# Optimization experiments

Measured on AMD Instinct MI355X. Metric: run time of the kernel, lower is better.

Reference implementation:

```python
import jax, jax.numpy as jnp
import numpy as np
import math

GROUPS = 32
EPS = 1e-5

def group_norm(x, w, b):
    B, C, H, W = x.shape
    xg = x.reshape(B, GROUPS, C // GROUPS, H, W)
    mu = xg.mean(axis=(2, 3, 4), keepdims=True)
    var = xg.var(axis=(2, 3, 4), keepdims=True)
    xn = ((xg - mu) * jax.lax.rsqrt(var + EPS)).reshape(B, C, H, W)
    return xn * w[None, :, None, None] + b[None, :, None, None]

def conv1x1(x, w, b):
    # x: [B,Cin,H,W], w: [Cout,Cin], b: [Cout]
    return jnp.einsum('bchw,oc->bohw', x, w) + b[None, :, None, None]

def setup_inputs() -> dict:
    key = jax.random.key(0)
    ks = jax.random.split(key, 8)
    B, C, E, H, W = 8, 256, 512, 64, 64
    x = jax.random.normal(ks[0], (B, C, H, W), dtype=jnp.float32)
    condA = jax.random.normal(ks[1], (B, E, H, W), dtype=jnp.float32)
    gn_x_w = jnp.ones((C,), jnp.float32)
    gn_x_b = jnp.zeros((C,), jnp.float32)
    gn_c_w = jnp.ones((E,), jnp.float32)
    gn_c_b = jnp.zeros((E,), jnp.float32)
    q_w = jax.random.normal(ks[2], (C, C), jnp.float32) * 0.02
    q_b = jnp.zeros((C,), jnp.float32)
    k_w = jax.random.normal(ks[3], (C, E), jnp.float32) * 0.02
    k_b = jnp.zeros((C,), jnp.float32)
    v_w = jax.random.normal(ks[4], (C, E), jnp.float32) * 0.02
    v_b = jnp.zeros((C,), jnp.float32)
    return {"x": x, "condA": condA, "gn_x_w": gn_x_w, "gn_x_b": gn_x_b,
            "gn_c_w": gn_c_w, "gn_c_b": gn_c_b, "q_w": q_w, "q_b": q_b,
            "k_w": k_w, "k_b": k_b, "v_w": v_w, "v_b": v_b}

def reference(x, condA, gn_x_w, gn_x_b, gn_c_w, gn_c_b, q_w, q_b, k_w, k_b, v_w, v_b):
    B, C, H, W = x.shape
    scale = math.sqrt(C)
    h = group_norm(x, gn_x_w, gn_x_b)
    h1 = group_norm(condA, gn_c_w, gn_c_b)
    q = conv1x1(h, q_w, q_b)      # [B,C,H,W]
    k = conv1x1(h1, k_w, k_b)     # [B,C,Hc,Wc]
    v = conv1x1(h1, v_w, v_b)     # [B,C,Hc,Wc]
    qf = q.transpose(0, 2, 3, 1).reshape(B, H * W, C)        # [B,N,C]
    kf = k.reshape(B, C, -1)                                  # [B,C,M]
    vf = v.transpose(0, 2, 3, 1).reshape(B, -1, C)            # [B,M,C]
    attn = jax.nn.softmax(jnp.einsum('bnc,bcm->bnm', qf, kf) / scale, axis=-1)
    out = jnp.einsum('bnm,bmc->bnc', attn, vf)                # [B,N,C]
    return out.reshape(B, H, W, C).transpose(0, 3, 1, 2)
```

## Files before the change

### kernel.cpp

```cpp
#include <hip/hip_runtime.h>


typedef _Float16 half8 __attribute__((ext_vector_type(8)));
typedef _Float16 half4v __attribute__((ext_vector_type(4)));
typedef float f32x4 __attribute__((ext_vector_type(4)));
typedef float f32x16 __attribute__((ext_vector_type(16)));

#define MFMA16(a, b, c) __builtin_amdgcn_mfma_f32_16x16x32_f16((a), (b), (c), 0, 0, 0)
#define MFMA32(a, b, c) __builtin_amdgcn_mfma_f32_32x32x16_f16((a), (b), (c), 0, 0, 0)

__global__ __launch_bounds__(256) void statswconv_kernel(
    const float* __restrict__ x, const float* __restrict__ condA,
    float* __restrict__ sx, float* __restrict__ sc,
    const float* __restrict__ wq, const float* __restrict__ wk,
    const float* __restrict__ wv, _Float16* __restrict__ wqt,
    _Float16* __restrict__ wkt, _Float16* __restrict__ wvt) {
  int bid = blockIdx.x;
  int t = threadIdx.x;
  if (bid >= 512) {
    int i = (bid - 512) * 256 + t;
    const float* src;
    _Float16* dst;
    int cin, ksbits, gi;
    if (i < 8192) { src = wq; dst = wqt; cin = 256; ksbits = 3; gi = i; }
    else if (i < 24576) { src = wk; dst = wkt; cin = 512; ksbits = 4; gi = i - 8192; }
    else { src = wv; dst = wvt; cin = 512; ksbits = 4; gi = i - 24576; }
    int tile = gi >> 6, g = gi & 63;
    int otile = tile >> ksbits, ks = tile & ((1 << ksbits) - 1);
    int o = otile * 16 + (g & 15), k = ks * 32 + (g >> 4) * 8;
    const float* s = src + (size_t)o * cin + k;
    half8 hv;
#pragma unroll
    for (int j = 0; j < 8; j++) hv[j] = (_Float16)s[j];
    *(half8*)(dst + (size_t)gi * 8) = hv;
    return;
  }
  const float4* src;
  int nf4;
  float* dst;
  float inv_n;
  if (bid < 256) {
    src = (const float4*)(x + (size_t)bid * 32768);
    nf4 = 8192;
    dst = sx + bid * 2;
    inv_n = 1.0f / 32768.0f;
  } else {
    int j = bid - 256;
    src = (const float4*)(condA + (size_t)j * 65536);
    nf4 = 16384;
    dst = sc + j * 2;
    inv_n = 1.0f / 65536.0f;
  }
  float s = 0.f, s2 = 0.f;
  for (int i = t; i < nf4; i += 256) {
    float4 v = src[i];
    s += v.x + v.y + v.z + v.w;
    s2 += v.x * v.x + v.y * v.y + v.z * v.z + v.w * v.w;
  }
#pragma unroll
  for (int m = 1; m <= 32; m <<= 1) {
    s += __shfl_xor(s, m, 64);
    s2 += __shfl_xor(s2, m, 64);
  }
  __shared__ float red[8];
  int w = t >> 6;
  if ((t & 63) == 0) { red[w * 2] = s; red[w * 2 + 1] = s2; }
  __syncthreads();
  if (t == 0) {
    float S = red[0] + red[2] + red[4] + red[6];
    float S2 = red[1] + red[3] + red[5] + red[7];
    float mu = S * inv_n;
    float var = S2 * inv_n - mu * mu;
    dst[0] = mu;
    dst[1] = rsqrtf(var + 1e-5f);
  }
}

__global__ __launch_bounds__(256) void ntrans_kernel(
    const float* __restrict__ x, const float* __restrict__ condA,
    const float* __restrict__ statsx, const float* __restrict__ statsc,
    const float* __restrict__ gxw, const float* __restrict__ gxb,
    const float* __restrict__ gcw, const float* __restrict__ gcb,
    _Float16* __restrict__ hxTt, _Float16* __restrict__ h1Tt) {
  int bid = blockIdx.x;
  const float *src, *stats, *gw, *gb;
  _Float16* dst;
  int CH, gsh, bid2;
  if (bid < 2048) {
    src = x; stats = statsx; gw = gxw; gb = gxb; dst = hxTt;
    CH = 256; gsh = 3; bid2 = bid;
  } else {
    src = condA; stats = statsc; gw = gcw; gb = gcb; dst = h1Tt;
    CH = 512; gsh = 4; bid2 = bid - 2048;
  }
  int b = bid2 & 7, nt = (bid2 >> 3) & 63, ctile = bid2 >> 9;
  int n0 = nt * 64, c0 = ctile * 64;
  int t = threadIdx.x;
  __shared__ float tile[64][65];

  int cl = t >> 2;
  int c = c0 + cl;
  const float* st = stats + ((size_t)b * 32 + (c >> gsh)) * 2;
  float mu = st[0], rs = st[1];
  float a = rs * gw[c];
  float bb = gb[c] - mu * a;
  const float* srow = src + ((size_t)(b * CH + c)) * 4096 + n0 + (t & 3) * 16;
#pragma unroll
  for (int i = 0; i < 4; i++) {
    float4 v = *(const float4*)(srow + 4 * i);
    int nn = (t & 3) * 16 + 4 * i;
    tile[cl][nn + 0] = v.x * a + bb;
    tile[cl][nn + 1] = v.y * a + bb;
    tile[cl][nn + 2] = v.z * a + bb;
    tile[cl][nn + 3] = v.w * a + bb;
  }
  __syncthreads();
  int nl = t >> 2;
  half8 ov[2];
#pragma unroll
  for (int u = 0; u < 2; u++)
#pragma unroll
    for (int i = 0; i < 8; i++) ov[u][i] = (_Float16)tile[(t & 3) * 16 + 8 * u + i][nl];
  int n = n0 + nl;
  size_t tb = ((size_t)b * 256 + (n >> 4)) * (CH >> 5);
  int ca = c0 + (t & 3) * 16;
#pragma unroll
  for (int u = 0; u < 2; u++) {
    int cc = ca + 8 * u;
    size_t addr = ((tb + (cc >> 5)) * 64 + (n & 15) + 16 * ((cc >> 3) & 3)) * 8;
    *(half8*)(dst + addr) = ov[u];
  }
}

__global__ __launch_bounds__(256, 2) void projQ_kernel(
    const _Float16* __restrict__ Ht, const _Float16* __restrict__ Wt,
    const float* __restrict__ bias, _Float16* __restrict__ Qt) {
  int bid = blockIdx.x;
  int b = bid & 7, nt = bid >> 3;
  int t = threadIdx.x, l = t & 63, w = t >> 6;
  int c15 = l & 15, q = l >> 4;

  __shared__ __align__(16) _Float16 hbuf[16384];
  half8* hb = (half8*)hbuf;
  {
    const half8* sg = (const half8*)Ht + (size_t)(b * 256 + nt * 4) * 512;
#pragma unroll
    for (int i = 0; i < 8; i++) hb[t + 256 * i] = sg[t + 256 * i];
  }
  __syncthreads();

  const half8* wt8 = (const half8*)Wt;
#pragma unroll
  for (int p = 0; p < 2; p++) {
    int oa = (p * 4 + w) * 2;
    f32x4 acc[2][4] = {};
#pragma unroll
    for (int ks = 0; ks < 8; ks++) {
      half8 af0 = wt8[((size_t)(oa + 0) * 8 + ks) * 64 + l];
      half8 af1 = wt8[((size_t)(oa + 1) * 8 + ks) * 64 + l];
#pragma unroll
      for (int nt2 = 0; nt2 < 4; nt2++) {
        half8 bf = hb[(nt2 * 8 + ks) * 64 + l];
        acc[0][nt2] = MFMA16(af0, bf, acc[0][nt2]);
        acc[1][nt2] = MFMA16(af1, bf, acc[1][nt2]);
      }
    }
#pragma unroll
    for (int j = 0; j < 2; j++) {
      int o4 = (oa + j) * 16 + 4 * q;
      f32x4 bv = *(const f32x4*)(bias + o4);
#pragma unroll
      for (int nt2 = 0; nt2 < 4; nt2++) {
        half4v hv;
#pragma unroll
        for (int r = 0; r < 4; r++) hv[r] = (_Float16)((acc[j][nt2][r] + bv[r]) * 0.0625f);
        size_t addr = ((((size_t)b * 128 + nt * 2 + (nt2 >> 1)) * 16 + (oa + j)) * 64 +
                       (nt2 & 1) * 16 + c15 + 32 * (q >> 1)) * 8 + (q & 1) * 4;
        *(half4v*)(Qt + addr) = hv;
      }
    }
  }
}

__global__ __launch_bounds__(256, 2) void projKV_kernel(
    const _Float16* __restrict__ Ht, const _Float16* __restrict__ Wk,
    const _Float16* __restrict__ Wv, const float* __restrict__ kb,
    const float* __restrict__ vb, _Float16* __restrict__ Kt,
    _Float16* __restrict__ Vt) {
  int bid = blockIdx.x;
  int b = bid & 7, mt = bid >> 3;
  int m0 = mt * 64;
  int t = threadIdx.x, l = t & 63, w = t >> 6;
  int c15 = l & 15, q = l >> 4;

  __shared__ __align__(16) _Float16 hbuf[32768];
  half8* hb = (half8*)hbuf;
  {
    const half8* sg = (const half8*)Ht + (size_t)(b * 256 + mt * 4) * 1024;
#pragma unroll
    for (int i = 0; i < 16; i++) hb[t + 256 * i] = sg[t + 256 * i];
  }
  __syncthreads();

  const half8* wk8 = (const half8*)Wk;
  const half8* wv8 = (const half8*)Wv;
#pragma unroll
  for (int p = 0; p < 2; p++) {
    int oa = (p * 4 + w) * 2;
    f32x4 acck[2][4] = {};
    f32x4 accv[4][2] = {};
#pragma unroll
    for (int ks = 0; ks < 16; ks++) {
      half8 kf0 = wk8[((size_t)(oa + 0) * 16 + ks) * 64 + l];
      half8 kf1 = wk8[((size_t)(oa + 1) * 16 + ks) * 64 + l];
      half8 vf0 = wv8[((size_t)(oa + 0) * 16 + ks) * 64 + l];
      half8 vf1 = wv8[((size_t)(oa + 1) * 16 + ks) * 64 + l];
#pragma unroll
      for (int nt2 = 0; nt2 < 4; nt2++) {
        half8 lf = hb[(nt2 * 16 + ks) * 64 + l];
        acck[0][nt2] = MFMA16(kf0, lf, acck[0][nt2]);
        acck[1][nt2] = MFMA16(kf1, lf, acck[1][nt2]);
        accv[nt2][0] = MFMA16(lf, vf0, accv[nt2][0]);
        accv[nt2][1] = MFMA16(lf, vf1, accv[nt2][1]);
      }
    }
#pragma unroll
    for (int j = 0; j < 2; j++) {
      int o4 = (oa + j) * 16 + 4 * q;
      f32x4 bv = *(const f32x4*)(kb + o4);
#pragma unroll
      for (int nt2 = 0; nt2 < 4; nt2++) {
        half4v hv;
#pragma unroll
        for (int r = 0; r < 4; r++) hv[r] = (_Float16)(acck[j][nt2][r] + bv[r]);
        size_t addr = ((((size_t)b * 128 + mt * 2 + (nt2 >> 1)) * 16 + (oa + j)) * 64 +
                       (nt2 & 1) * 16 + c15 + 32 * (q >> 1)) * 8 + (q & 1) * 4;
        *(half4v*)(Kt + addr) = hv;
      }
    }
#pragma unroll
    for (int nt2 = 0; nt2 < 4; nt2++) {
      int m = m0 + nt2 * 16 + 4 * q;
      size_t mbase = ((size_t)b * 256 + (m >> 4)) * 8;
#pragma unroll
      for (int j = 0; j < 2; j++) {
        int c = (oa + j) * 16 + c15;
        float bs = vb[c];
        half4v hv;
#pragma unroll
        for (int r = 0; r < 4; r++) hv[r] = (_Float16)(accv[nt2][j][r] + bs);
        size_t addr = ((mbase + (c >> 5)) * 64 + (c & 31) + ((q >> 1) << 5)) * 8 + (q & 1) * 4;
        *(half4v*)(Vt + addr) = hv;
      }
    }
  }
}

__global__ __launch_bounds__(256, 2) void attn_kernel(
    const _Float16* __restrict__ Qt, const _Float16* __restrict__ Kt,
    const _Float16* __restrict__ Vt, float* __restrict__ out,
    float* __restrict__ O1, float* __restrict__ l0g,
    float* __restrict__ l1g) {
  int bid = blockIdx.x;
  int b = bid & 7, nt = (bid >> 3) & 63, ms = bid >> 9;
  int n0 = nt * 64;
  int t = threadIdx.x, l = t & 63, w = t >> 6;
  int l31 = l & 31, h = l >> 5;
  int mh = w & 1, nh = w >> 1;
  int it0 = ms * 32, it1 = it0 + 32;

  __shared__ __align__(16) _Float16 pbuf[8192];
  float* lsw = (float*)pbuf;

  half8 qf[16];
  {
    const half8* qt8 = (const half8*)Qt + ((size_t)(b * 128 + nt * 2 + nh) * 16) * 64 + l;
#pragma unroll
    for (int ks = 0; ks < 16; ks++) qf[ks] = qt8[ks * 64];
  }

  const half8* kt8 = (const half8*)Kt + (size_t)b * 131072 + (size_t)(mh * 16) * 64 + l;
  const half8* vt8 = (const half8*)Vt + (size_t)b * 131072 + l;
  int gb = (l31 ^ h) | (h << 5);

  f32x16 acc_o[4] = {};
  float l_part = 0.f;

  for (int it = it0; it < it1; it++) {
    _Float16* pb = pbuf + (it & 1) * 4096;

    half8 kfA[8];
#pragma unroll
    for (int i = 0; i < 8; i++) kfA[i] = kt8[(size_t)it * 2048 + i * 64];
    half8 vf0[8];
#pragma unroll
    for (int u = 0; u < 2; u++)
#pragma unroll
      for (int ct = 0; ct < 4; ct++)
        vf0[u * 4 + ct] = vt8[((size_t)(it * 4 + u) * 8 + (mh * 4 + ct)) * 64];

    f32x16 s = {};
    __builtin_amdgcn_s_setprio(1);
#pragma unroll
    for (int ks = 0; ks < 8; ks++) s = MFMA32(kfA[ks], qf[ks], s);
    __builtin_amdgcn_s_setprio(0);
    half8 kfB[8];
#pragma unroll
    for (int i = 0; i < 8; i++) kfB[i] = kt8[(size_t)it * 2048 + (8 + i) * 64];
    __builtin_amdgcn_s_setprio(1);
#pragma unroll
    for (int ks = 0; ks < 8; ks++) s = MFMA32(kfB[ks], qf[8 + ks], s);
    __builtin_amdgcn_s_setprio(0);

    half4v pv[4];
#pragma unroll
    for (int k2 = 0; k2 < 4; k2++) {
#pragma unroll
      for (int r = 0; r < 4; r++) {
        float e = __expf(s[4 * k2 + r]);
        l_part += e;
        pv[k2][r] = (_Float16)e;
      }
    }

#pragma unroll
    for (int k2 = 0; k2 < 4; k2++) {
      int hm = k2 & 1;
      int tau = nh * 4 + mh * 2 + (k2 >> 1);
      int g = (l31 ^ hm) | (hm << 5);
      *(half4v*)&pb[tau * 512 + g * 8 + 4 * h] = pv[k2];
    }
    __syncthreads();

    half8 vf1[8];
#pragma unroll
    for (int u = 0; u < 2; u++)
#pragma unroll
      for (int ct = 0; ct < 4; ct++)
        vf1[u * 4 + ct] = vt8[((size_t)(it * 4 + 2 + u) * 8 + (mh * 4 + ct)) * 64];
    __builtin_amdgcn_s_setprio(1);
#pragma unroll
    for (int ks = 0; ks < 2; ks++) {
      half8 pf = *(const half8*)&pb[(nh * 4 + ks) * 512 + gb * 8];
#pragma unroll
      for (int ct = 0; ct < 4; ct++) acc_o[ct] = MFMA32(pf, vf0[ks * 4 + ct], acc_o[ct]);
    }
#pragma unroll
    for (int ks = 2; ks < 4; ks++) {
      half8 pf = *(const half8*)&pb[(nh * 4 + ks) * 512 + gb * 8];
#pragma unroll
      for (int ct = 0; ct < 4; ct++) acc_o[ct] = MFMA32(pf, vf1[(ks - 2) * 4 + ct], acc_o[ct]);
    }
    __builtin_amdgcn_s_setprio(0);
  }

  __syncthreads();
  {
    float v = l_part + __shfl_xor(l_part, 32, 64);
    if (l < 32) lsw[mh * 64 + nh * 32 + l] = v;
  }
  __syncthreads();
  float* obase = ms ? O1 : out;
#pragma unroll
  for (int k2 = 0; k2 < 4; k2++) {
    int nb = nh * 32 + 4 * h + 8 * k2;
#pragma unroll
    for (int ct = 0; ct < 4; ct++) {
      int c = mh * 128 + ct * 32 + l31;
      f32x4 o4;
#pragma unroll
      for (int r = 0; r < 4; r++) o4[r] = acc_o[ct][4 * k2 + r];
      *(f32x4*)(obase + ((size_t)(b * 256 + c)) * 4096 + n0 + nb) = o4;
    }
  }
  if (t < 64) {
    float* lG = ms ? l1g : l0g;
    lG[b * 4096 + n0 + t] = lsw[t] + lsw[64 + t];
  }
}

__global__ __launch_bounds__(256) void combine_kernel(
    float* __restrict__ out, const float* __restrict__ O1,
    const float* __restrict__ l0g, const float* __restrict__ l1g) {
  size_t i = (size_t)blockIdx.x * 256 + threadIdx.x;
  f32x4 a = ((const f32x4*)out)[i];
  f32x4 b4 = ((const f32x4*)O1)[i];
  int bidx = (int)(i >> 18);
  int n4 = (int)(i & 1023);
  f32x4 La = ((const f32x4*)l0g)[bidx * 1024 + n4];
  f32x4 Lb = ((const f32x4*)l1g)[bidx * 1024 + n4];
  f32x4 r;
#pragma unroll
  for (int j = 0; j < 4; j++) r[j] = (a[j] + b4[j]) / (La[j] + Lb[j]);
  ((f32x4*)out)[i] = r;
}

extern "C" void kernel_launch(void* const* d_in, const int* in_sizes, int n_in,
                              void* d_out, int out_size, void* d_ws,
                              size_t ws_size, hipStream_t stream) {
  const float* x = (const float*)d_in[0];
  const float* condA = (const float*)d_in[1];
  const float* gxw = (const float*)d_in[2];
  const float* gxb = (const float*)d_in[3];
  const float* gcw = (const float*)d_in[4];
  const float* gcb = (const float*)d_in[5];
  const float* qw = (const float*)d_in[6];
  const float* qb = (const float*)d_in[7];
  const float* kw = (const float*)d_in[8];
  const float* kb = (const float*)d_in[9];
  const float* vw = (const float*)d_in[10];
  const float* vb = (const float*)d_in[11];
  float* out = (float*)d_out;

  char* ws = (char*)d_ws;
  float* statsx = (float*)(ws);
  float* statsc = (float*)(ws + 2048);
  _Float16* wqt = (_Float16*)(ws + 4096);
  _Float16* wkt = (_Float16*)(ws + 135168);
  _Float16* wvt = (_Float16*)(ws + 397312);
  char* p = ws + 659456;
  _Float16* hxTt = (_Float16*)p; p += (size_t)8 * 4096 * 256 * 2;
  _Float16* h1Tt = (_Float16*)p; p += (size_t)8 * 4096 * 512 * 2;
  _Float16* Qt = (_Float16*)p;   p += (size_t)8 * 4096 * 256 * 2;
  _Float16* Kt = (_Float16*)p;   p += (size_t)8 * 4096 * 256 * 2;
  _Float16* Vt = (_Float16*)p;

  float* O1 = (float*)(ws + 659456);
  float* l0g = (float*)(ws + 659456 + (size_t)33554432);
  float* l1g = (float*)(ws + 659456 + (size_t)33554432 + 131072);

  statswconv_kernel<<<672, 256, 0, stream>>>(x, condA, statsx, statsc,
                                             qw, kw, vw, wqt, wkt, wvt);
  ntrans_kernel<<<6144, 256, 0, stream>>>(x, condA, statsx, statsc,
                                          gxw, gxb, gcw, gcb, hxTt, h1Tt);
  projQ_kernel<<<512, 256, 0, stream>>>(hxTt, wqt, qb, Qt);
  projKV_kernel<<<512, 256, 0, stream>>>(h1Tt, wkt, wvt, kb, vb, Kt, Vt);
  attn_kernel<<<1024, 256, 0, stream>>>(Qt, Kt, Vt, out, O1, l0g, l1g);
  combine_kernel<<<8192, 256, 0, stream>>>(out, O1, l0g, l1g);
}
```

Before: 421.5 us.

## Restructure attention to split keys across waves and pass P via permlane

The attention kernel drops the two-block split over the key range. Instead, each block covers all 64 key tiles, and the two wave halves (mh) each take half of every key tile and write separate partial outputs for the combine kernel to merge. Q is staged once into LDS and read per k-step rather than kept in registers. The exp'd P tile now moves from the QK accumulator layout into the PV operand layout with v_permlane32_swap, which removes the LDS round trip and the per-iteration __syncthreads. The cost is half as many blocks, 8 f32x16 accumulators per wave (more register pressure), and extra LDS reads of Q on every iteration.

```diff
diff --git a/kernel.cpp b/kernel.cpp
--- a/kernel.cpp
+++ b/kernel.cpp
@@ -3,8 +3,10 @@
 
 typedef _Float16 half8 __attribute__((ext_vector_type(8)));
 typedef _Float16 half4v __attribute__((ext_vector_type(4)));
+typedef _Float16 half2v __attribute__((ext_vector_type(2)));
 typedef float f32x4 __attribute__((ext_vector_type(4)));
 typedef float f32x16 __attribute__((ext_vector_type(16)));
+typedef unsigned u32x4v __attribute__((ext_vector_type(4)));
 
 #define MFMA16(a, b, c) __builtin_amdgcn_mfma_f32_16x16x32_f16((a), (b), (c), 0, 0, 0)
 #define MFMA32(a, b, c) __builtin_amdgcn_mfma_f32_32x32x16_f16((a), (b), (c), 0, 0, 0)
@@ -262,120 +264,103 @@
     float* __restrict__ O1, float* __restrict__ l0g,
     float* __restrict__ l1g) {
   int bid = blockIdx.x;
-  int b = bid & 7, nt = (bid >> 3) & 63, ms = bid >> 9;
+  int b = bid & 7, nt = bid >> 3;
   int n0 = nt * 64;
   int t = threadIdx.x, l = t & 63, w = t >> 6;
   int l31 = l & 31, h = l >> 5;
   int mh = w & 1, nh = w >> 1;
-  int it0 = ms * 32, it1 = it0 + 32;
-
-  __shared__ __align__(16) _Float16 pbuf[8192];
-  float* lsw = (float*)pbuf;
-
-  half8 qf[16];
+
+  __shared__ __align__(16) _Float16 qlds[16384];
+  half8* ql8 = (half8*)qlds;
   {
-    const half8* qt8 = (const half8*)Qt + ((size_t)(b * 128 + nt * 2 + nh) * 16) * 64 + l;
-#pragma unroll
-    for (int ks = 0; ks < 16; ks++) qf[ks] = qt8[ks * 64];
-  }
-
-  const half8* kt8 = (const half8*)Kt + (size_t)b * 131072 + (size_t)(mh * 16) * 64 + l;
+    const half8* sg = (const half8*)Qt + (size_t)(b * 128 + nt * 2) * 1024;
+#pragma unroll
+    for (int i = 0; i < 8; i++) ql8[t + 256 * i] = sg[t + 256 * i];
+  }
+  __syncthreads();
+
+  const half8* kt8 = (const half8*)Kt + (size_t)b * 131072 + mh * 1024 + l;
   const half8* vt8 = (const half8*)Vt + (size_t)b * 131072 + l;
-  int gb = (l31 ^ h) | (h << 5);
-
-  f32x16 acc_o[4] = {};
+  const half8* qw8 = ql8 + nh * 1024 + l;
+
+  f32x16 acc[8] = {};
   float l_part = 0.f;
 
-  for (int it = it0; it < it1; it++) {
-    _Float16* pb = pbuf + (it & 1) * 4096;
-
-    half8 kfA[8];
-#pragma unroll
-    for (int i = 0; i < 8; i++) kfA[i] = kt8[(size_t)it * 2048 + i * 64];
-    half8 vf0[8];
-#pragma unroll
-    for (int u = 0; u < 2; u++)
-#pragma unroll
-      for (int ct = 0; ct < 4; ct++)
-        vf0[u * 4 + ct] = vt8[((size_t)(it * 4 + u) * 8 + (mh * 4 + ct)) * 64];
+  for (int it = 0; it < 64; it++) {
+    const half8* kb = kt8 + (size_t)it * 2048;
 
     f32x16 s = {};
-    __builtin_amdgcn_s_setprio(1);
-#pragma unroll
-    for (int ks = 0; ks < 8; ks++) s = MFMA32(kfA[ks], qf[ks], s);
-    __builtin_amdgcn_s_setprio(0);
-    half8 kfB[8];
-#pragma unroll
-    for (int i = 0; i < 8; i++) kfB[i] = kt8[(size_t)it * 2048 + (8 + i) * 64];
-    __builtin_amdgcn_s_setprio(1);
-#pragma unroll
-    for (int ks = 0; ks < 8; ks++) s = MFMA32(kfB[ks], qf[8 + ks], s);
-    __builtin_amdgcn_s_setprio(0);
-
-    half4v pv[4];
-#pragma unroll
-    for (int k2 = 0; k2 < 4; k2++) {
-#pragma unroll
-      for (int r = 0; r < 4; r++) {
-        float e = __expf(s[4 * k2 + r]);
-        l_part += e;
-        pv[k2][r] = (_Float16)e;
-      }
-    }
-
-#pragma unroll
-    for (int k2 = 0; k2 < 4; k2++) {
-      int hm = k2 & 1;
-      int tau = nh * 4 + mh * 2 + (k2 >> 1);
-      int g = (l31 ^ hm) | (hm << 5);
-      *(half4v*)&pb[tau * 512 + g * 8 + 4 * h] = pv[k2];
-    }
-    __syncthreads();
-
-    half8 vf1[8];
-#pragma unroll
-    for (int u = 0; u < 2; u++)
-#pragma unroll
-      for (int ct = 0; ct < 4; ct++)
-        vf1[u * 4 + ct] = vt8[((size_t)(it * 4 + 2 + u) * 8 + (mh * 4 + ct)) * 64];
-    __builtin_amdgcn_s_setprio(1);
-#pragma unroll
-    for (int ks = 0; ks < 2; ks++) {
-      half8 pf = *(const half8*)&pb[(nh * 4 + ks) * 512 + gb * 8];
-#pragma unroll
-      for (int ct = 0; ct < 4; ct++) acc_o[ct] = MFMA32(pf, vf0[ks * 4 + ct], acc_o[ct]);
-    }
-#pragma unroll
-    for (int ks = 2; ks < 4; ks++) {
-      half8 pf = *(const half8*)&pb[(nh * 4 + ks) * 512 + gb * 8];
-#pragma unroll
-      for (int ct = 0; ct < 4; ct++) acc_o[ct] = MFMA32(pf, vf1[(ks - 2) * 4 + ct], acc_o[ct]);
-    }
-    __builtin_amdgcn_s_setprio(0);
-  }
-
-  __syncthreads();
+#pragma unroll
+    for (int g = 0; g < 4; g++) {
+      half8 kf[4], qb[4];
+#pragma unroll
+      for (int i = 0; i < 4; i++) kf[i] = kb[(g * 4 + i) * 64];
+#pragma unroll
+      for (int i = 0; i < 4; i++) qb[i] = qw8[(g * 4 + i) * 64];
+      __builtin_amdgcn_s_setprio(1);
+#pragma unroll
+      for (int i = 0; i < 4; i++) s = MFMA32(kf[i], qb[i], s);
+      __builtin_amdgcn_s_setprio(0);
+    }
+
+    unsigned uo[8];
+#pragma unroll
+    for (int k2 = 0; k2 < 8; k2++) {
+      float e0 = __expf(s[2 * k2]);
+      float e1 = __expf(s[2 * k2 + 1]);
+      l_part += e0 + e1;
+      half2v h2 = {(_Float16)e0, (_Float16)e1};
+      uo[k2] = __builtin_bit_cast(unsigned, h2);
+    }
+    unsigned x0 = uo[0], y0 = uo[2];
+    asm("v_permlane32_swap_b32 %0, %1" : "+v"(x0), "+v"(y0));
+    unsigned x1 = uo[1], y1 = uo[3];
+    asm("v_permlane32_swap_b32 %0, %1" : "+v"(x1), "+v"(y1));
+    unsigned x2 = uo[4], y2 = uo[6];
+    asm("v_permlane32_swap_b32 %0, %1" : "+v"(x2), "+v"(y2));
+    unsigned x3 = uo[5], y3 = uo[7];
+    asm("v_permlane32_swap_b32 %0, %1" : "+v"(x3), "+v"(y3));
+    u32x4v P0 = {x0, x1, y0, y1};
+    u32x4v P1 = {x2, x3, y2, y3};
+    half8 pf0 = __builtin_bit_cast(half8, P0);
+    half8 pf1 = __builtin_bit_cast(half8, P1);
+
+    const half8* vb0 = vt8 + (size_t)((it * 4 + mh * 2) * 8) * 64;
+#pragma unroll
+    for (int u = 0; u < 2; u++) {
+      const half8* vb = vb0 + u * 512;
+      half8 pfu = u ? pf1 : pf0;
+#pragma unroll
+      for (int g = 0; g < 2; g++) {
+        half8 vf[4];
+#pragma unroll
+        for (int i = 0; i < 4; i++) vf[i] = vb[(g * 4 + i) * 64];
+        __builtin_amdgcn_s_setprio(1);
+#pragma unroll
+        for (int i = 0; i < 4; i++)
+          acc[g * 4 + i] = MFMA32(pfu, vf[i], acc[g * 4 + i]);
+        __builtin_amdgcn_s_setprio(0);
+      }
+    }
+  }
+
   {
     float v = l_part + __shfl_xor(l_part, 32, 64);
-    if (l < 32) lsw[mh * 64 + nh * 32 + l] = v;
-  }
-  __syncthreads();
-  float* obase = ms ? O1 : out;
-#pragma unroll
-  for (int k2 = 0; k2 < 4; k2++) {
-    int nb = nh * 32 + 4 * h + 8 * k2;
-#pragma unroll
-    for (int ct = 0; ct < 4; ct++) {
-      int c = mh * 128 + ct * 32 + l31;
+    float* lG = mh ? l1g : l0g;
+    if (l < 32) lG[b * 4096 + n0 + nh * 32 + l] = v;
+  }
+  float* ob = mh ? O1 : out;
+#pragma unroll
+  for (int cb = 0; cb < 8; cb++) {
+    int c = cb * 32 + l31;
+    float* orow = ob + ((size_t)(b * 256 + c)) * 4096 + n0 + nh * 32 + 4 * h;
+#pragma unroll
+    for (int k2 = 0; k2 < 4; k2++) {
       f32x4 o4;
 #pragma unroll
-      for (int r = 0; r < 4; r++) o4[r] = acc_o[ct][4 * k2 + r];
-      *(f32x4*)(obase + ((size_t)(b * 256 + c)) * 4096 + n0 + nb) = o4;
-    }
-  }
-  if (t < 64) {
-    float* lG = ms ? l1g : l0g;
-    lG[b * 4096 + n0 + t] = lsw[t] + lsw[64 + t];
+      for (int r = 0; r < 4; r++) o4[r] = acc[cb][4 * k2 + r];
+      *(f32x4*)(orow + 8 * k2) = o4;
+    }
   }
 }
 
@@ -435,6 +420,6 @@
                                           gxw, gxb, gcw, gcb, hxTt, h1Tt);
   projQ_kernel<<<512, 256, 0, stream>>>(hxTt, wqt, qb, Qt);
   projKV_kernel<<<512, 256, 0, stream>>>(h1Tt, wkt, wvt, kb, vb, Kt, Vt);
-  attn_kernel<<<1024, 256, 0, stream>>>(Qt, Kt, Vt, out, O1, l0g, l1g);
+  attn_kernel<<<512, 256, 0, stream>>>(Qt, Kt, Vt, out, O1, l0g, l1g);
   combine_kernel<<<8192, 256, 0, stream>>>(out, O1, l0g, l1g);
 }
```

After: 411.0 us. -2.5%, faster.
